# Optimization experiments

Measured on AMD Instinct MI355X. Metric: run time of the kernel, lower is better.

Reference implementation:

```python
import jax, jax.numpy as jnp
import numpy as np

B, C, E, L = 32, 64, 512, 100


def setup_inputs() -> dict:
    key = jax.random.key(0)
    k1, k2, k3, k4, k5, k6 = jax.random.split(key, 6)
    scale = 1.0 / np.sqrt(E)
    return {
        "c_emb": jax.random.normal(k1, (B, C, E), dtype=jnp.float32),
        "c_pred": jax.random.uniform(k2, (B, C), dtype=jnp.float32),
        "W1": jax.random.normal(k3, (L, E, E), dtype=jnp.float32) * scale,
        "b1": jax.random.normal(k4, (L, E), dtype=jnp.float32) * scale,
        "W2": jax.random.normal(k5, (L, E), dtype=jnp.float32) * scale,
        "b2": jax.random.normal(k6, (L,), dtype=jnp.float32) * scale,
    }


def reference(c_emb, c_pred, W1, b1, W2, b2):
    # Per-label 2-layer MLP weight generator, batched across all L labels.
    # h: [B, C, L, E]  -- hidden of Linear(E,E)+ReLU for every label
    h = jax.nn.relu(jnp.einsum('bce,leh->bclh', c_emb, W1) + b1[None, None, :, :])
    # w: [B, C, L]     -- second Linear(E,1) per label -> generated concept weights
    w = jnp.einsum('bclh,lh->bcl', h, W2) + b2[None, None, :]
    # logits[:, :, i] = weights_i * c_pred ; y[:, i] = sum_c c_pred * weights_i (bmm)
    logits = w * c_pred[:, :, None]          # [B, C, L]
    y = jnp.sum(logits, axis=1)              # [B, L]
    return (y, logits)
```

## Files before the change

kernel.cpp:

```cpp
#include <hip/hip_runtime.h>


typedef unsigned short u16;
typedef unsigned int   u32;
typedef __attribute__((ext_vector_type(8))) short short8;
typedef __attribute__((ext_vector_type(4))) float f32x4;
typedef __attribute__((address_space(1))) const u32 as1_u32;
typedef __attribute__((address_space(3))) u32 as3_u32;

#define E_DIM 512
#define L_DIM 100
#define Y_SZ  3200
#define LG_OFF 3200

__device__ __forceinline__ u16 f2bf(float f) {
  union { float f; u32 u; } v; v.f = f;
  u32 u = v.u;
  u32 r = u + 0x7fffu + ((u >> 16) & 1u);
  return (u16)(r >> 16);
}

__global__ __launch_bounds__(256) void conv_a_kernel(const float* __restrict__ src,
                                                     u16* __restrict__ dst) {
  int g = blockIdx.x * 256 + threadIdx.x;
  int base = g << 3;
  int bc = base >> 9;
  int e  = base & 511;
  const float4* p = (const float4*)(src + base);
  float4 v0 = p[0];
  float4 v1 = p[1];
  union { u16 h[8]; uint4 q; } u;
  u.h[0]=f2bf(v0.x); u.h[1]=f2bf(v0.y); u.h[2]=f2bf(v0.z); u.h[3]=f2bf(v0.w);
  u.h[4]=f2bf(v1.x); u.h[5]=f2bf(v1.y); u.h[6]=f2bf(v1.z); u.h[7]=f2bf(v1.w);
  int mt = bc >> 7, kt = e >> 6, r = bc & 127, c = e & 63;
  int idx = (mt*8 + kt)*8192 + r*64 + (c ^ ((r & 7) << 3));
  *(uint4*)(dst + idx) = u.q;
}

__global__ __launch_bounds__(256) void conv_w_kernel(const float* __restrict__ W1,
                                                     u16* __restrict__ dst) {
  __shared__ float T[64][65];
  int blk = blockIdx.x;
  int l = blk >> 6;
  int rem = blk & 63;
  int et = rem >> 3, ht = rem & 7;
  int tid = threadIdx.x;
  int e0 = et*64, h0 = ht*64;
  const float* basep = W1 + (size_t)l * (E_DIM*E_DIM);
  int erow = tid >> 4;
  int hq = (tid & 15) * 4;
  #pragma unroll
  for (int i = 0; i < 4; ++i) {
    int e = erow + i*16;
    float4 v = *(const float4*)(basep + (size_t)(e0 + e)*E_DIM + h0 + hq);
    T[e][hq+0] = v.x; T[e][hq+1] = v.y; T[e][hq+2] = v.z; T[e][hq+3] = v.w;
  }
  __syncthreads();
  int rl_h = tid >> 3;
  int c0 = (tid & 7) * 8;
  size_t tbase = ((size_t)(l*4 + (ht >> 1))*8 + et) * 8192;
  #pragma unroll
  for (int p = 0; p < 2; ++p) {
    int r_local = p*32 + rl_h;
    union { u16 h[8]; uint4 q; } u;
    #pragma unroll
    for (int j = 0; j < 8; ++j) u.h[j] = f2bf(T[c0 + j][r_local]);
    int r = ((ht & 1) << 6) + r_local;
    size_t idx = tbase + r*64 + (c0 ^ ((r & 7) << 3));
    *(uint4*)(dst + idx) = u.q;
  }
}

__global__ __launch_bounds__(256, 2) void gemm_kernel(
    const u16* __restrict__ Aws, const u16* __restrict__ Wws,
    const float* __restrict__ c_pred, const float* __restrict__ b1,
    const float* __restrict__ W2, const float* __restrict__ b2,
    float* __restrict__ out)
{
  __shared__ __align__(16) u16 As[2][8192];
  __shared__ __align__(16) u16 Bs[2][8192];

  const int wg  = blockIdx.x;
  const int swz = (wg & 7) * 200 + (wg >> 3);
  const int l   = swz >> 4;
  const int mt  = swz & 15;
  const int tid = threadIdx.x;
  const int wid = tid >> 6;
  const int lane = tid & 63;
  const int wr = wid >> 1;
  const int wc = wid & 1;
  const int lr = lane & 15;
  const int lgp = lane >> 4;

  float wacc[4][4];
  #pragma unroll
  for (int m = 0; m < 4; ++m)
    #pragma unroll
    for (int r = 0; r < 4; ++r) wacc[m][r] = 0.f;

  auto stage = [&](int buf, int hb, int kt) {
    const u16* asrc = Aws + (mt*8 + kt)*8192;
    const u16* bsrc = Wws + ((l*4 + hb)*8 + kt)*8192;
    #pragma unroll
    for (int i = 0; i < 4; ++i) {
      int chunk = wid*4 + i;
      int uoff = chunk*512;
      int goff = uoff + lane*8;
      __builtin_amdgcn_global_load_lds((as1_u32*)(asrc + goff),
                                       (as3_u32*)(&As[buf][uoff]), 16, 0, 0);
      __builtin_amdgcn_global_load_lds((as1_u32*)(bsrc + goff),
                                       (as3_u32*)(&Bs[buf][uoff]), 16, 0, 0);
    }
  };

  stage(0, 0, 0);
  __syncthreads();
  int cur = 0;
  const f32x4 zero4 = {0.f, 0.f, 0.f, 0.f};

  for (int hb = 0; hb < 4; ++hb) {
    f32x4 acc[4][4];
    #pragma unroll
    for (int mi = 0; mi < 4; ++mi)
      #pragma unroll
      for (int ni = 0; ni < 4; ++ni) acc[mi][ni] = zero4;

    for (int kt = 0; kt < 8; ++kt) {
      int nkt = kt + 1, nhb = hb;
      if (nkt == 8) { nkt = 0; ++nhb; }
      if (nhb < 4) stage(cur ^ 1, nhb, nkt);

      #pragma unroll
      for (int ks = 0; ks < 2; ++ks) {
        short8 af[4], bfr[4];
        #pragma unroll
        for (int mi = 0; mi < 4; ++mi) {
          int row = wr*64 + mi*16 + lr;
          int col = ks*32 + lgp*8;
          af[mi] = *(const short8*)&As[cur][row*64 + (col ^ ((row & 7) << 3))];
        }
        #pragma unroll
        for (int ni = 0; ni < 4; ++ni) {
          int row = wc*64 + ni*16 + lr;
          int col = ks*32 + lgp*8;
          bfr[ni] = *(const short8*)&Bs[cur][row*64 + (col ^ ((row & 7) << 3))];
        }
        #pragma unroll
        for (int mi = 0; mi < 4; ++mi)
          #pragma unroll
          for (int ni = 0; ni < 4; ++ni)
            acc[mi][ni] = __builtin_amdgcn_mfma_f32_16x16x32_bf16(
                af[mi], bfr[ni], acc[mi][ni], 0, 0, 0);
      }
      __syncthreads();
      cur ^= 1;
    }

    #pragma unroll
    for (int ni = 0; ni < 4; ++ni) {
      int h = hb*128 + wc*64 + ni*16 + lr;
      float b1v = b1[l*E_DIM + h];
      float w2v = W2[l*E_DIM + h];
      #pragma unroll
      for (int mi = 0; mi < 4; ++mi)
        #pragma unroll
        for (int r = 0; r < 4; ++r) {
          float v = acc[mi][ni][r] + b1v;
          v = fmaxf(v, 0.f);
          wacc[mi][r] = fmaf(v, w2v, wacc[mi][r]);
        }
    }
  }

  #pragma unroll
  for (int m = 0; m < 4; ++m)
    #pragma unroll
    for (int r = 0; r < 4; ++r) {
      float s = wacc[m][r];
      s += __shfl_xor(s, 1);
      s += __shfl_xor(s, 2);
      s += __shfl_xor(s, 4);
      s += __shfl_xor(s, 8);
      wacc[m][r] = s;
    }

  float (*w_part)[128] = (float(*)[128])&As[0][0];
  if (lr == 0) {
    #pragma unroll
    for (int m = 0; m < 4; ++m)
      #pragma unroll
      for (int r = 0; r < 4; ++r)
        w_part[wc][wr*64 + m*16 + lgp*4 + r] = wacc[m][r];
  }
  __syncthreads();

  if (tid < 128) {
    int bcg = mt*128 + tid;
    float w = w_part[0][tid] + w_part[1][tid] + b2[l];
    float lgt = w * c_pred[bcg];
    out[LG_OFF + bcg*L_DIM + l] = lgt;
    float s = lgt;
    s += __shfl_down(s, 32);
    s += __shfl_down(s, 16);
    s += __shfl_down(s, 8);
    s += __shfl_down(s, 4);
    s += __shfl_down(s, 2);
    s += __shfl_down(s, 1);
    if (lane == 0) out[(bcg >> 6)*L_DIM + l] = s;
  }
}

__global__ __launch_bounds__(256) void naive_kernel(
    const float* __restrict__ c_emb, const float* __restrict__ c_pred,
    const float* __restrict__ W1, const float* __restrict__ b1,
    const float* __restrict__ W2, const float* __restrict__ b2,
    float* __restrict__ out)
{
  __shared__ float a_lds[16][512];
  __shared__ float wsum[4][16];
  int l = blockIdx.y;
  int rt = blockIdx.x;
  int tid = threadIdx.x, lane = tid & 63, wid = tid >> 6;
  int row0 = rt * 16;
  #pragma unroll
  for (int i = 0; i < 8; ++i) {
    int flat = i*1024 + tid*4;
    int r = flat >> 9, e = flat & 511;
    *(float4*)&a_lds[r][e] = *(const float4*)&c_emb[(size_t)(row0 + r)*E_DIM + e];
  }
  __syncthreads();
  int h0 = tid, h1 = tid + 256;
  const float* w1b = W1 + (size_t)l * (E_DIM*E_DIM);
  float acc0[16], acc1[16];
  #pragma unroll
  for (int r = 0; r < 16; ++r) { acc0[r] = 0.f; acc1[r] = 0.f; }
  for (int e = 0; e < E_DIM; ++e) {
    float wa = w1b[(size_t)e*E_DIM + h0];
    float wb = w1b[(size_t)e*E_DIM + h1];
    #pragma unroll
    for (int r = 0; r < 16; ++r) {
      float a = a_lds[r][e];
      acc0[r] = fmaf(a, wa, acc0[r]);
      acc1[r] = fmaf(a, wb, acc1[r]);
    }
  }
  float b1a = b1[l*E_DIM + h0], b1c = b1[l*E_DIM + h1];
  float w2a = W2[l*E_DIM + h0], w2c = W2[l*E_DIM + h1];
  float part[16];
  #pragma unroll
  for (int r = 0; r < 16; ++r) {
    float v0 = fmaxf(acc0[r] + b1a, 0.f) * w2a;
    float v1 = fmaxf(acc1[r] + b1c, 0.f) * w2c;
    part[r] = v0 + v1;
  }
  #pragma unroll
  for (int r = 0; r < 16; ++r) {
    float s = part[r];
    s += __shfl_down(s, 32); s += __shfl_down(s, 16); s += __shfl_down(s, 8);
    s += __shfl_down(s, 4);  s += __shfl_down(s, 2);  s += __shfl_down(s, 1);
    if (lane == 0) wsum[wid][r] = s;
  }
  __syncthreads();
  if (tid < 16) {
    float w = wsum[0][tid] + wsum[1][tid] + wsum[2][tid] + wsum[3][tid] + b2[l];
    int bc = row0 + tid;
    float lgt = w * c_pred[bc];
    out[LG_OFF + bc*L_DIM + l] = lgt;
    atomicAdd(&out[(bc >> 6)*L_DIM + l], lgt);
  }
}

extern "C" void kernel_launch(void* const* d_in, const int* in_sizes, int n_in,
                              void* d_out, int out_size, void* d_ws, size_t ws_size,
                              hipStream_t stream) {
  const float* c_emb  = (const float*)d_in[0];
  const float* c_pred = (const float*)d_in[1];
  const float* W1     = (const float*)d_in[2];
  const float* b1     = (const float*)d_in[3];
  const float* W2     = (const float*)d_in[4];
  const float* b2     = (const float*)d_in[5];
  float* out = (float*)d_out;

  const size_t nA = 1048576;
  const size_t nW = 26214400;
  const size_t need = 2*nA + 2*nW;

  if (ws_size >= need) {
    u16* Aws = (u16*)d_ws;
    u16* Wws = (u16*)d_ws + nA;
    conv_a_kernel<<<512, 256, 0, stream>>>(c_emb, Aws);
    conv_w_kernel<<<6400, 256, 0, stream>>>(W1, Wws);
    gemm_kernel<<<1600, 256, 0, stream>>>(Aws, Wws, c_pred, b1, W2, b2, out);
  } else {
    hipMemsetAsync(out, 0, Y_SZ*sizeof(float), stream);
    naive_kernel<<<dim3(128, 100), 256, 0, stream>>>(c_emb, c_pred, W1, b1, W2, b2, out);
  }
}
```

Baseline: 323.8 us.

## Enlarge GEMM tile to 256x256 with 512 threads and half-K pipelined staging

Each GEMM workgroup now covers 256 rows by 256 hidden columns using 8 waves (instead of 128x128 with 4 waves). The conversion kernels write a new half-K-split swizzled workspace layout to match. The main loop is reorganised into 16 virtual K-tiles, each staged as two 32-wide halves, with explicit vmcnt waits and raw s_barrier so loads overlap the MFMA work. The goal is more operand reuse per LDS byte, less global traffic per FLOP and fewer workgroups, at the cost of more accumulator registers and more LDS (64 KB per workgroup), which may lower occupancy.

Result: slower. 992.3 us (+206.5%).

```diff
diff --git a/kernel.cpp b/kernel.cpp
--- a/kernel.cpp
+++ b/kernel.cpp
@@ -32,8 +32,10 @@
   union { u16 h[8]; uint4 q; } u;
   u.h[0]=f2bf(v0.x); u.h[1]=f2bf(v0.y); u.h[2]=f2bf(v0.z); u.h[3]=f2bf(v0.w);
   u.h[4]=f2bf(v1.x); u.h[5]=f2bf(v1.y); u.h[6]=f2bf(v1.z); u.h[7]=f2bf(v1.w);
-  int mt = bc >> 7, kt = e >> 6, r = bc & 127, c = e & 63;
-  int idx = (mt*8 + kt)*8192 + r*64 + (c ^ ((r & 7) << 3));
+  int mt = bc >> 8, row = bc & 255;
+  int kt = e >> 6, ks = (e >> 5) & 1, bp = (e >> 3) & 3;
+  int s = (row >> 1) & 3;
+  int idx = ((mt*8 + kt)*2 + ks)*8192 + row*32 + ((bp ^ s) << 3);
   *(uint4*)(dst + idx) = u.q;
 }
 
@@ -58,145 +60,157 @@
   __syncthreads();
   int rl_h = tid >> 3;
   int c0 = (tid & 7) * 8;
-  size_t tbase = ((size_t)(l*4 + (ht >> 1))*8 + et) * 8192;
+  int ks = c0 >> 5, bp = (c0 >> 3) & 3;
   #pragma unroll
   for (int p = 0; p < 2; ++p) {
     int r_local = p*32 + rl_h;
     union { u16 h[8]; uint4 q; } u;
     #pragma unroll
     for (int j = 0; j < 8; ++j) u.h[j] = f2bf(T[c0 + j][r_local]);
-    int r = ((ht & 1) << 6) + r_local;
-    size_t idx = tbase + r*64 + (c0 ^ ((r & 7) << 3));
+    int hgl = h0 + r_local;
+    int nb = hgl >> 8, row = hgl & 255;
+    int s = (row >> 1) & 3;
+    size_t idx = (size_t)((((l*2 + nb)*8 + et)*2 + ks))*8192
+               + row*32 + ((bp ^ s) << 3);
     *(uint4*)(dst + idx) = u.q;
   }
 }
 
-__global__ __launch_bounds__(256, 2) void gemm_kernel(
+__global__ __launch_bounds__(512, 2) void gemm_kernel(
     const u16* __restrict__ Aws, const u16* __restrict__ Wws,
     const float* __restrict__ c_pred, const float* __restrict__ b1,
     const float* __restrict__ W2, const float* __restrict__ b2,
     float* __restrict__ out)
 {
-  __shared__ __align__(16) u16 As[2][8192];
-  __shared__ __align__(16) u16 Bs[2][8192];
+  __shared__ __align__(16) u16 As[2][2][8192];
+  __shared__ __align__(16) u16 Bs[2][2][8192];
 
   const int wg  = blockIdx.x;
-  const int swz = (wg & 7) * 200 + (wg >> 3);
-  const int l   = swz >> 4;
-  const int mt  = swz & 15;
+  const int swzid = (wg & 7) * 100 + (wg >> 3);
+  const int l   = swzid >> 3;
+  const int mt  = swzid & 7;
   const int tid = threadIdx.x;
   const int wid = tid >> 6;
   const int lane = tid & 63;
-  const int wr = wid >> 1;
-  const int wc = wid & 1;
+  const int wr = wid >> 2;
+  const int wn = wid & 3;
   const int lr = lane & 15;
   const int lgp = lane >> 4;
 
-  float wacc[4][4];
-  #pragma unroll
-  for (int m = 0; m < 4; ++m)
-    #pragma unroll
-    for (int r = 0; r < 4; ++r) wacc[m][r] = 0.f;
-
-  auto stage = [&](int buf, int hb, int kt) {
-    const u16* asrc = Aws + (mt*8 + kt)*8192;
-    const u16* bsrc = Wws + ((l*4 + hb)*8 + kt)*8192;
-    #pragma unroll
-    for (int i = 0; i < 4; ++i) {
-      int chunk = wid*4 + i;
-      int uoff = chunk*512;
-      int goff = uoff + lane*8;
-      __builtin_amdgcn_global_load_lds((as1_u32*)(asrc + goff),
-                                       (as3_u32*)(&As[buf][uoff]), 16, 0, 0);
-      __builtin_amdgcn_global_load_lds((as1_u32*)(bsrc + goff),
-                                       (as3_u32*)(&Bs[buf][uoff]), 16, 0, 0);
-    }
+  float b1v0[4], w2v0[4], b1v1[4], w2v1[4];
+  #pragma unroll
+  for (int ni = 0; ni < 4; ++ni) {
+    int h = wn*64 + ni*16 + lr;
+    b1v0[ni] = b1[l*E_DIM + h];        w2v0[ni] = W2[l*E_DIM + h];
+    b1v1[ni] = b1[l*E_DIM + 256 + h];  w2v1[ni] = W2[l*E_DIM + 256 + h];
+  }
+
+  const int rA = wr*128 + lr;
+  const int aU = rA*32 + ((lgp ^ ((rA >> 1) & 3)) << 3);
+  const int rB = wn*64 + lr;
+  const int bU = rB*32 + ((lgp ^ ((rB >> 1) & 3)) << 3);
+
+  auto stage = [&](int vt, int ks) {
+    const int kt = vt & 7, nb = vt >> 3, pp = vt & 1;
+    const u16* asrc = Aws + (size_t)((mt*8 + kt)*2 + ks)*8192 + wid*1024 + lane*8;
+    const u16* bsrc = Wws + (size_t)(((l*2 + nb)*8 + kt)*2 + ks)*8192 + wid*1024 + lane*8;
+    u16* ad = &As[pp][ks][wid*1024];
+    u16* bd = &Bs[pp][ks][wid*1024];
+    __builtin_amdgcn_global_load_lds((as1_u32*)asrc,       (as3_u32*)ad,       16, 0, 0);
+    __builtin_amdgcn_global_load_lds((as1_u32*)(asrc+512), (as3_u32*)(ad+512), 16, 0, 0);
+    __builtin_amdgcn_global_load_lds((as1_u32*)bsrc,       (as3_u32*)bd,       16, 0, 0);
+    __builtin_amdgcn_global_load_lds((as1_u32*)(bsrc+512), (as3_u32*)(bd+512), 16, 0, 0);
   };
 
-  stage(0, 0, 0);
-  __syncthreads();
-  int cur = 0;
-  const f32x4 zero4 = {0.f, 0.f, 0.f, 0.f};
-
-  for (int hb = 0; hb < 4; ++hb) {
-    f32x4 acc[4][4];
-    #pragma unroll
-    for (int mi = 0; mi < 4; ++mi)
+  f32x4 acc[8][4];
+  #pragma unroll
+  for (int mi = 0; mi < 8; ++mi)
+    #pragma unroll
+    for (int ni = 0; ni < 4; ++ni) acc[mi][ni] = (f32x4){0.f,0.f,0.f,0.f};
+  float wacc[8][4];
+  #pragma unroll
+  for (int mi = 0; mi < 8; ++mi)
+    #pragma unroll
+    for (int r = 0; r < 4; ++r) wacc[mi][r] = 0.f;
+
+  auto compute = [&](int pp, int ks) {
+    short8 af[8], bf[4];
+    #pragma unroll
+    for (int ni = 0; ni < 4; ++ni)
+      bf[ni] = *(const short8*)&Bs[pp][ks][bU + ni*512];
+    #pragma unroll
+    for (int mi = 0; mi < 8; ++mi)
+      af[mi] = *(const short8*)&As[pp][ks][aU + mi*512];
+    #pragma unroll
+    for (int mi = 0; mi < 8; ++mi)
       #pragma unroll
-      for (int ni = 0; ni < 4; ++ni) acc[mi][ni] = zero4;
-
-    for (int kt = 0; kt < 8; ++kt) {
-      int nkt = kt + 1, nhb = hb;
-      if (nkt == 8) { nkt = 0; ++nhb; }
-      if (nhb < 4) stage(cur ^ 1, nhb, nkt);
-
+      for (int ni = 0; ni < 4; ++ni)
+        acc[mi][ni] = __builtin_amdgcn_mfma_f32_16x16x32_bf16(
+            af[mi], bf[ni], acc[mi][ni], 0, 0, 0);
+  };
+
+  auto fold = [&](const float* b1v, const float* w2v) {
+    #pragma unroll
+    for (int mi = 0; mi < 8; ++mi)
       #pragma unroll
-      for (int ks = 0; ks < 2; ++ks) {
-        short8 af[4], bfr[4];
-        #pragma unroll
-        for (int mi = 0; mi < 4; ++mi) {
-          int row = wr*64 + mi*16 + lr;
-          int col = ks*32 + lgp*8;
-          af[mi] = *(const short8*)&As[cur][row*64 + (col ^ ((row & 7) << 3))];
-        }
-        #pragma unroll
-        for (int ni = 0; ni < 4; ++ni) {
-          int row = wc*64 + ni*16 + lr;
-          int col = ks*32 + lgp*8;
-          bfr[ni] = *(const short8*)&Bs[cur][row*64 + (col ^ ((row & 7) << 3))];
-        }
-        #pragma unroll
-        for (int mi = 0; mi < 4; ++mi)
-          #pragma unroll
-          for (int ni = 0; ni < 4; ++ni)
-            acc[mi][ni] = __builtin_amdgcn_mfma_f32_16x16x32_bf16(
-                af[mi], bfr[ni], acc[mi][ni], 0, 0, 0);
-      }
-      __syncthreads();
-      cur ^= 1;
-    }
-
-    #pragma unroll
-    for (int ni = 0; ni < 4; ++ni) {
-      int h = hb*128 + wc*64 + ni*16 + lr;
-      float b1v = b1[l*E_DIM + h];
-      float w2v = W2[l*E_DIM + h];
-      #pragma unroll
-      for (int mi = 0; mi < 4; ++mi)
+      for (int ni = 0; ni < 4; ++ni)
         #pragma unroll
         for (int r = 0; r < 4; ++r) {
-          float v = acc[mi][ni][r] + b1v;
-          v = fmaxf(v, 0.f);
-          wacc[mi][r] = fmaf(v, w2v, wacc[mi][r]);
+          float v = fmaxf(acc[mi][ni][r] + b1v[ni], 0.f);
+          wacc[mi][r] = fmaf(v, w2v[ni], wacc[mi][r]);
+          acc[mi][ni][r] = 0.f;
         }
-    }
-  }
-
-  #pragma unroll
-  for (int m = 0; m < 4; ++m)
+  };
+
+  stage(0, 0); stage(0, 1);
+
+  for (int vt = 0; vt < 16; ++vt) {
+    const int pp = vt & 1;
+    if (vt < 15) { stage(vt+1, 0); asm volatile("s_waitcnt vmcnt(8)" ::: "memory"); }
+    else         {                 asm volatile("s_waitcnt vmcnt(4)" ::: "memory"); }
+    __builtin_amdgcn_sched_barrier(0);
+    __builtin_amdgcn_s_barrier();
+    __builtin_amdgcn_sched_barrier(0);
+    compute(pp, 0);
+    if (vt < 15) { stage(vt+1, 1); asm volatile("s_waitcnt vmcnt(8)" ::: "memory"); }
+    else         {                 asm volatile("s_waitcnt vmcnt(0)" ::: "memory"); }
+    __builtin_amdgcn_sched_barrier(0);
+    __builtin_amdgcn_s_barrier();
+    __builtin_amdgcn_sched_barrier(0);
+    compute(pp, 1);
+    if (vt == 7)       fold(b1v0, w2v0);
+    else if (vt == 15) fold(b1v1, w2v1);
+  }
+
+  __syncthreads();
+
+  #pragma unroll
+  for (int mi = 0; mi < 8; ++mi)
     #pragma unroll
     for (int r = 0; r < 4; ++r) {
-      float s = wacc[m][r];
+      float s = wacc[mi][r];
       s += __shfl_xor(s, 1);
       s += __shfl_xor(s, 2);
       s += __shfl_xor(s, 4);
       s += __shfl_xor(s, 8);
-      wacc[m][r] = s;
+      wacc[mi][r] = s;
     }
 
-  float (*w_part)[128] = (float(*)[128])&As[0][0];
+  float (*w_part)[256] = (float(*)[256])&As[0][0][0];
   if (lr == 0) {
     #pragma unroll
-    for (int m = 0; m < 4; ++m)
+    for (int mi = 0; mi < 8; ++mi)
       #pragma unroll
       for (int r = 0; r < 4; ++r)
-        w_part[wc][wr*64 + m*16 + lgp*4 + r] = wacc[m][r];
-  }
-  __syncthreads();
-
-  if (tid < 128) {
-    int bcg = mt*128 + tid;
-    float w = w_part[0][tid] + w_part[1][tid] + b2[l];
+        w_part[wn][wr*128 + mi*16 + lgp*4 + r] = wacc[mi][r];
+  }
+  __syncthreads();
+
+  if (tid < 256) {
+    int row = tid;
+    float w = w_part[0][row] + w_part[1][row] + w_part[2][row] + w_part[3][row]
+            + b2[l];
+    int bcg = mt*256 + row;
     float lgt = w * c_pred[bcg];
     out[LG_OFF + bcg*L_DIM + l] = lgt;
     float s = lgt;
@@ -290,7 +304,7 @@
     u16* Wws = (u16*)d_ws + nA;
     conv_a_kernel<<<512, 256, 0, stream>>>(c_emb, Aws);
     conv_w_kernel<<<6400, 256, 0, stream>>>(W1, Wws);
-    gemm_kernel<<<1600, 256, 0, stream>>>(Aws, Wws, c_pred, b1, W2, b2, out);
+    gemm_kernel<<<800, 512, 0, stream>>>(Aws, Wws, c_pred, b1, W2, b2, out);
   } else {
     hipMemsetAsync(out, 0, Y_SZ*sizeof(float), stream);
     naive_kernel<<<dim3(128, 100), 256, 0, stream>>>(c_emb, c_pred, W1, b1, W2, b2, out);
```
